# Kernel tuning notes

Hardware: AMD Instinct MI355X
Metric: run time of the kernel (lower is better)

## Reference

```python
import jax, jax.numpy as jnp
import numpy as np

N_LEVELS = 8
BASE_RES = 16
LOG2_T = 14
T = 1 << LOG2_T
WIDTH, HEIGHT = 1024, 768
NUM_GAUSSIAN = 8
PRIME_Y = np.uint32(2654435761)
CORNERS = np.array([[0, 0], [1, 0], [0, 1], [1, 1]], dtype=np.uint32)


def _level_resolutions():
    bx = np.exp((np.log(WIDTH) - np.log(BASE_RES)) / (N_LEVELS - 1))
    by = np.exp((np.log(HEIGHT) - np.log(BASE_RES)) / (N_LEVELS - 1))
    return [(int(np.floor(BASE_RES * bx ** l)), int(np.floor(BASE_RES * by ** l)))
            for l in range(N_LEVELS)]


def hash_encode(x, hashidxs, table):
    # x: [N,2] in [0,1]; hashidxs: [N] int; table: [V, L, T, 2]
    feats = []
    offs = jnp.asarray(CORNERS)  # [4,2] uint32
    hv = hashidxs.astype(jnp.int32)[:, None]  # [N,1]
    for l, (rx, ry) in enumerate(_level_resolutions()):
        res = jnp.array([rx, ry], dtype=x.dtype)
        pos = x * res                      # [N,2]
        p0 = jnp.floor(pos)
        w = pos - p0                       # bilinear weights, [N,2]
        c = p0.astype(jnp.uint32)[:, None, :] + offs[None]  # [N,4,2]
        h = (c[..., 0] * jnp.uint32(1)) ^ (c[..., 1] * PRIME_Y)
        idx = (h & jnp.uint32(T - 1)).astype(jnp.int32)      # [N,4]
        f = table[hv, l, idx]              # [N,4,2] gather per corner
        wx, wy = w[:, 0:1], w[:, 1:2]
        ww = jnp.concatenate([(1 - wx) * (1 - wy), wx * (1 - wy),
                              (1 - wx) * wy, wx * wy], axis=1)  # [N,4]
        feats.append(jnp.sum(f * ww[..., None], axis=1))        # [N,2]
    return jnp.concatenate(feats, axis=-1)  # [N,16]


def gaussian_act(x, sigma=0.1):
    return jnp.exp(x * x * (-1.0 / (2.0 * sigma * sigma)))


def setup_inputs() -> dict:
    key = jax.random.key(0)
    ks = jax.random.split(key, 8)
    N = 2 ** 21
    V = 20
    x = jax.random.uniform(ks[0], (N, 2), dtype=jnp.float32)
    hashidxs = jax.random.randint(ks[1], (N,), 0, V, dtype=jnp.int32)
    color = jax.random.uniform(ks[2], (N, 3), dtype=jnp.float32)
    table = jax.random.normal(ks[3], (V, N_LEVELS, T, 2), dtype=jnp.float32) * 1e-2
    w1 = jax.random.normal(ks[4], (16, 32), dtype=jnp.float32) * (1.0 / np.sqrt(16))
    b1 = jax.random.normal(ks[5], (32,), dtype=jnp.float32) * 0.01
    w2 = jax.random.normal(ks[6], (32, 3 * NUM_GAUSSIAN), dtype=jnp.float32) * (1.0 / np.sqrt(32))
    b2 = jax.random.normal(ks[7], (3 * NUM_GAUSSIAN,), dtype=jnp.float32) * 0.01
    return {"x": x, "hashidxs": hashidxs, "color": color, "table": table,
            "w1": w1, "b1": b1, "w2": w2, "b2": b2}


def reference(x, hashidxs, color, table, w1, b1, w2, b2):
    H = hash_encode(x, hashidxs, table)            # [N,16]
    h1 = gaussian_act(H @ w1 + b1)                 # [N,32]
    raw = h1 @ w2 + b2                             # [N,24]
    G = NUM_GAUSSIAN
    weight = jnp.exp(raw[..., :G])
    mu = jax.nn.sigmoid(raw[..., G:2 * G])
    inv_sigma = jnp.exp(raw[..., 2 * G:3 * G])
    return mu, inv_sigma, weight, H
```

## Files before the change

kernel.cpp:

```cpp
#include <hip/hip_runtime.h>
#include <cmath>

#define NLEV 8
#define TSZ 16384
#define PRIME 2654435761u
#define NBINS 32

typedef float fx2 __attribute__((ext_vector_type(2)));

struct Res { int rx[NLEV]; int ry[NLEV]; };

__device__ __forceinline__ void compute_point(
    fx2 xv, int hv, int p,
    const float* __restrict__ table,
    const float* __restrict__ w1, const float* __restrict__ b1,
    const float* __restrict__ w2, const float* __restrict__ b2,
    float* __restrict__ out, int N, const Res& res)
{
    const float* tb_base = table + (size_t)hv * (NLEV * TSZ * 2);

    float H[16];
    #pragma unroll
    for (int l = 0; l < NLEV; ++l) {
        float fx = (float)res.rx[l], fy = (float)res.ry[l];
        float posx = xv.x * fx, posy = xv.y * fy;
        float p0x = floorf(posx), p0y = floorf(posy);
        float wx = posx - p0x, wy = posy - p0y;
        unsigned cx = (unsigned)p0x, cy = (unsigned)p0y;
        const float* tb = tb_base + (size_t)l * (TSZ * 2);
        unsigned hy0 = cy * PRIME;
        unsigned hy1 = (cy + 1u) * PRIME;
        unsigned i00 = ( cx        ^ hy0) & (TSZ - 1);
        unsigned i10 = ((cx + 1u)  ^ hy0) & (TSZ - 1);
        unsigned i01 = ( cx        ^ hy1) & (TSZ - 1);
        unsigned i11 = ((cx + 1u)  ^ hy1) & (TSZ - 1);
        fx2 f00 = *(const fx2*)(tb + 2u * i00);
        fx2 f10 = *(const fx2*)(tb + 2u * i10);
        fx2 f01 = *(const fx2*)(tb + 2u * i01);
        fx2 f11 = *(const fx2*)(tb + 2u * i11);
        float w00 = (1.f - wx) * (1.f - wy);
        float w10 = wx * (1.f - wy);
        float w01 = (1.f - wx) * wy;
        float w11 = wx * wy;
        H[2*l]   = fmaf(f00.x, w00, fmaf(f10.x, w10, fmaf(f01.x, w01, f11.x * w11)));
        H[2*l+1] = fmaf(f00.y, w00, fmaf(f10.y, w10, fmaf(f01.y, w01, f11.y * w11)));
    }

    float h1[32];
    #pragma unroll
    for (int j = 0; j < 32; ++j) {
        float s = b1[j];
        #pragma unroll
        for (int k = 0; k < 16; ++k) s = fmaf(H[k], w1[k * 32 + j], s);
        h1[j] = __expf(-50.f * s * s);
    }

    float raw[24];
    #pragma unroll
    for (int j = 0; j < 24; ++j) {
        float s = b2[j];
        #pragma unroll
        for (int k = 0; k < 32; ++k) s = fmaf(h1[k], w2[k * 24 + j], s);
        raw[j] = s;
    }

    float wt[8], mu[8], isg[8];
    #pragma unroll
    for (int g = 0; g < 8; ++g) {
        wt[g]  = __expf(raw[g]);
        mu[g]  = 1.f / (1.f + __expf(-raw[8 + g]));
        isg[g] = __expf(raw[16 + g]);
    }

    size_t N8 = (size_t)N * 8;
    float4* o;
    o = (float4*)(out) + (size_t)p * 2;
    o[0] = make_float4(mu[0], mu[1], mu[2], mu[3]);
    o[1] = make_float4(mu[4], mu[5], mu[6], mu[7]);
    o = (float4*)(out + N8) + (size_t)p * 2;
    o[0] = make_float4(isg[0], isg[1], isg[2], isg[3]);
    o[1] = make_float4(isg[4], isg[5], isg[6], isg[7]);
    o = (float4*)(out + 2 * N8) + (size_t)p * 2;
    o[0] = make_float4(wt[0], wt[1], wt[2], wt[3]);
    o[1] = make_float4(wt[4], wt[5], wt[6], wt[7]);
    o = (float4*)(out + 3 * N8) + (size_t)p * 4;
    o[0] = make_float4(H[0],  H[1],  H[2],  H[3]);
    o[1] = make_float4(H[4],  H[5],  H[6],  H[7]);
    o[2] = make_float4(H[8],  H[9],  H[10], H[11]);
    o[3] = make_float4(H[12], H[13], H[14], H[15]);
}

__global__ __launch_bounds__(256) void pg_kernel(
    const float* __restrict__ x, const int* __restrict__ hashidxs,
    const float* __restrict__ table,
    const float* __restrict__ w1, const float* __restrict__ b1,
    const float* __restrict__ w2, const float* __restrict__ b2,
    float* __restrict__ out, int N, Res res)
{
    int i = blockIdx.x * blockDim.x + threadIdx.x;
    if (i >= N) return;
    fx2 xv = ((const fx2*)x)[i];
    int hv = hashidxs[i];
    compute_point(xv, hv, i, table, w1, b1, w2, b2, out, N, res);
}

__global__ void k_zero(int* __restrict__ c) {
    int t = threadIdx.x;
    if (t < 2 * NBINS) c[t] = 0;
}

__global__ __launch_bounds__(256) void k_hist(
    const int* __restrict__ hashidxs, int N, int* __restrict__ hist)
{
    __shared__ int lh[NBINS];
    int t = threadIdx.x;
    if (t < NBINS) lh[t] = 0;
    __syncthreads();
    int i = blockIdx.x * 256 + t;
    if (i < N) atomicAdd(&lh[hashidxs[i]], 1);
    __syncthreads();
    if (t < NBINS && lh[t]) atomicAdd(&hist[t], lh[t]);
}

__global__ void k_scan(const int* __restrict__ hist, int* __restrict__ cursor) {
    if (threadIdx.x == 0 && blockIdx.x == 0) {
        int acc = 0;
        for (int b = 0; b < NBINS; ++b) { cursor[b] = acc; acc += hist[b]; }
    }
}

__global__ __launch_bounds__(256) void k_scatter(
    const float* __restrict__ x, const int* __restrict__ hashidxs, int N,
    int* __restrict__ cursor, int* __restrict__ order, float* __restrict__ sx)
{
    __shared__ int lh[NBINS];
    __shared__ int lbase[NBINS];
    int t = threadIdx.x;
    if (t < NBINS) lh[t] = 0;
    __syncthreads();
    int i = blockIdx.x * 256 + t;
    int hv = -1, r = 0;
    if (i < N) { hv = hashidxs[i]; r = atomicAdd(&lh[hv], 1); }
    __syncthreads();
    if (t < NBINS && lh[t]) lbase[t] = atomicAdd(&cursor[t], lh[t]);
    __syncthreads();
    if (i < N) {
        int pos = lbase[hv] + r;
        order[pos] = i | (hv << 24);
        ((fx2*)sx)[pos] = ((const fx2*)x)[i];
    }
}

__global__ __launch_bounds__(256) void pg_main(
    const int*   __restrict__ order,
    const float* __restrict__ sx,
    const float* __restrict__ table,
    const float* __restrict__ w1, const float* __restrict__ b1,
    const float* __restrict__ w2, const float* __restrict__ b2,
    float* __restrict__ out, int N, Res res)
{
    unsigned nwg  = gridDim.x, orig = blockIdx.x;
    unsigned q = nwg / 8u, rr = nwg % 8u, xcd = orig % 8u;
    unsigned wg = (xcd < rr ? xcd * (q + 1u) : rr * (q + 1u) + (xcd - rr) * q) + orig / 8u;
    int j = (int)(wg * 256u + threadIdx.x);
    if (j >= N) return;

    int packed = order[j];
    int p  = packed & 0xFFFFFF;
    int hv = packed >> 24;
    fx2 xv = ((const fx2*)sx)[j];
    compute_point(xv, hv, p, table, w1, b1, w2, b2, out, N, res);
}

extern "C" void kernel_launch(void* const* d_in, const int* in_sizes, int n_in,
                              void* d_out, int out_size, void* d_ws, size_t ws_size,
                              hipStream_t stream) {
    const float* x        = (const float*)d_in[0];
    const int*   hashidxs = (const int*)  d_in[1];
    const float* table    = (const float*)d_in[3];
    const float* w1       = (const float*)d_in[4];
    const float* b1       = (const float*)d_in[5];
    const float* w2       = (const float*)d_in[6];
    const float* b2       = (const float*)d_in[7];
    float* out = (float*)d_out;
    int N = in_sizes[0] / 2;

    Res res;
    double bx = std::exp((std::log((double)1024) - std::log((double)16)) / 7.0);
    double by = std::exp((std::log((double)768)  - std::log((double)16)) / 7.0);
    for (int l = 0; l < NLEV; ++l) {
        res.rx[l] = (int)std::floor(16.0 * std::pow(bx, (double)l));
        res.ry[l] = (int)std::floor(16.0 * std::pow(by, (double)l));
    }

    dim3 block(256);
    unsigned nwg = (unsigned)((N + 255) / 256);
    dim3 grid(nwg);

    size_t order_off = 1024;
    size_t sx_off    = order_off + (((size_t)N * 4 + 255) & ~(size_t)255);
    size_t ws_need   = sx_off + (size_t)N * 8;

    if (ws_size < ws_need || N >= (1 << 24)) {
        hipLaunchKernelGGL(pg_kernel, grid, block, 0, stream,
                           x, hashidxs, table, w1, b1, w2, b2, out, N, res);
        return;
    }

    int*   hist   = (int*)d_ws;
    int*   cursor = (int*)d_ws + NBINS;
    int*   order  = (int*)((char*)d_ws + order_off);
    float* sx     = (float*)((char*)d_ws + sx_off);

    hipLaunchKernelGGL(k_zero,    dim3(1),   dim3(64),  0, stream, hist);
    hipLaunchKernelGGL(k_hist,    grid,      block,     0, stream, hashidxs, N, hist);
    hipLaunchKernelGGL(k_scan,    dim3(1),   dim3(32),  0, stream, hist, cursor);
    hipLaunchKernelGGL(k_scatter, grid,      block,     0, stream, x, hashidxs, N, cursor, order, sx);
    hipLaunchKernelGGL(pg_main,   grid,      block,     0, stream,
                       order, sx, table, w1, b1, w2, b2, out, N, res);
}
```

Before: 832.3 us.

## Sort points by hash table and spatial cell; pack MLP FMAs

Points were sorted only by hash-table index. They are now binned by table index and a 16x16 spatial cell, so neighbouring threads gather nearby hash-table entries and get better cache reuse. The histogram, scan and scatter kernels are generalised to thousands of bins, using dynamic LDS and a parallel block scan. The two MLP layers now use two-wide vector FMAs so the compiler can emit packed fp32 instructions. The cost is larger LDS use and more global atomics in the sort kernels.

```diff
diff --git a/kernel.cpp b/kernel.cpp
--- a/kernel.cpp
+++ b/kernel.cpp
@@ -4,7 +4,8 @@
 #define NLEV 8
 #define TSZ 16384
 #define PRIME 2654435761u
-#define NBINS 32
+#define CELLS 256
+#define MAXV 32
 
 typedef float fx2 __attribute__((ext_vector_type(2)));
 
@@ -46,23 +47,38 @@
         H[2*l+1] = fmaf(f00.y, w00, fmaf(f10.y, w10, fmaf(f01.y, w01, f11.y * w11)));
     }
 
+    fx2 acc1[16];
+    #pragma unroll
+    for (int j = 0; j < 16; ++j) acc1[j] = ((const fx2*)b1)[j];
+    #pragma unroll
+    for (int k = 0; k < 16; ++k) {
+        fx2 hk = {H[k], H[k]};
+        const fx2* wrow = (const fx2*)(w1 + k * 32);
+        #pragma unroll
+        for (int j = 0; j < 16; ++j)
+            acc1[j] = __builtin_elementwise_fma(hk, wrow[j], acc1[j]);
+    }
     float h1[32];
     #pragma unroll
-    for (int j = 0; j < 32; ++j) {
-        float s = b1[j];
+    for (int j = 0; j < 16; ++j) {
+        h1[2*j]   = __expf(-50.f * acc1[j].x * acc1[j].x);
+        h1[2*j+1] = __expf(-50.f * acc1[j].y * acc1[j].y);
+    }
+
+    fx2 acc2[12];
+    #pragma unroll
+    for (int j = 0; j < 12; ++j) acc2[j] = ((const fx2*)b2)[j];
+    #pragma unroll
+    for (int k = 0; k < 32; ++k) {
+        fx2 hk = {h1[k], h1[k]};
+        const fx2* wrow = (const fx2*)(w2 + k * 24);
         #pragma unroll
-        for (int k = 0; k < 16; ++k) s = fmaf(H[k], w1[k * 32 + j], s);
-        h1[j] = __expf(-50.f * s * s);
-    }
-
+        for (int j = 0; j < 12; ++j)
+            acc2[j] = __builtin_elementwise_fma(hk, wrow[j], acc2[j]);
+    }
     float raw[24];
     #pragma unroll
-    for (int j = 0; j < 24; ++j) {
-        float s = b2[j];
-        #pragma unroll
-        for (int k = 0; k < 32; ++k) s = fmaf(h1[k], w2[k * 24 + j], s);
-        raw[j] = s;
-    }
+    for (int j = 0; j < 12; ++j) { raw[2*j] = acc2[j].x; raw[2*j+1] = acc2[j].y; }
 
     float wt[8], mu[8], isg[8];
     #pragma unroll
@@ -104,50 +120,94 @@
     compute_point(xv, hv, i, table, w1, b1, w2, b2, out, N, res);
 }
 
-__global__ void k_zero(int* __restrict__ c) {
+__device__ __forceinline__ int spatial_bin(fx2 xv, int hv) {
+    int gx = (int)(xv.x * 16.f); gx = gx > 15 ? 15 : gx;
+    int gy = (int)(xv.y * 16.f); gy = gy > 15 ? 15 : gy;
+    return hv * CELLS + gy * 16 + gx;
+}
+
+__global__ __launch_bounds__(256) void k_zero(int* __restrict__ c, int n) {
+    int t = blockIdx.x * 256 + threadIdx.x;
+    if (t < n) c[t] = 0;
+}
+
+__global__ __launch_bounds__(256) void k_hist(
+    const float* __restrict__ x, const int* __restrict__ hashidxs, int N,
+    int* __restrict__ hist, int NB)
+{
+    extern __shared__ int lh[];
+    for (int b = threadIdx.x; b < NB; b += 256) lh[b] = 0;
+    __syncthreads();
+    int i = blockIdx.x * 256 + threadIdx.x;
+    if (i < N) atomicAdd(&lh[spatial_bin(((const fx2*)x)[i], hashidxs[i])], 1);
+    __syncthreads();
+    for (int b = threadIdx.x; b < NB; b += 256) {
+        int c = lh[b];
+        if (c) atomicAdd(&hist[b], c);
+    }
+}
+
+__global__ __launch_bounds__(256) void k_scan(
+    const int* __restrict__ hist, int* __restrict__ cursor, int NB)
+{
+    __shared__ int part[256];
     int t = threadIdx.x;
-    if (t < 2 * NBINS) c[t] = 0;
-}
-
-__global__ __launch_bounds__(256) void k_hist(
-    const int* __restrict__ hashidxs, int N, int* __restrict__ hist)
-{
-    __shared__ int lh[NBINS];
-    int t = threadIdx.x;
-    if (t < NBINS) lh[t] = 0;
-    __syncthreads();
-    int i = blockIdx.x * 256 + t;
-    if (i < N) atomicAdd(&lh[hashidxs[i]], 1);
-    __syncthreads();
-    if (t < NBINS && lh[t]) atomicAdd(&hist[t], lh[t]);
-}
-
-__global__ void k_scan(const int* __restrict__ hist, int* __restrict__ cursor) {
-    if (threadIdx.x == 0 && blockIdx.x == 0) {
-        int acc = 0;
-        for (int b = 0; b < NBINS; ++b) { cursor[b] = acc; acc += hist[b]; }
+    const int BPT = 32;
+    int loc[BPT];
+    int base = t * ((NB + 255) / 256);
+    int cnt  = (NB + 255) / 256;
+    int s = 0;
+    for (int b = 0; b < cnt; ++b) {
+        int bin = base + b;
+        loc[b] = s;
+        if (bin < NB) s += hist[bin];
+    }
+    part[t] = s;
+    __syncthreads();
+    #pragma unroll
+    for (int off = 1; off < 256; off <<= 1) {
+        int v = (t >= off) ? part[t - off] : 0;
+        __syncthreads();
+        part[t] += v;
+        __syncthreads();
+    }
+    int excl = (t == 0) ? 0 : part[t - 1];
+    for (int b = 0; b < cnt; ++b) {
+        int bin = base + b;
+        if (bin < NB) cursor[bin] = excl + loc[b];
     }
 }
 
 __global__ __launch_bounds__(256) void k_scatter(
     const float* __restrict__ x, const int* __restrict__ hashidxs, int N,
-    int* __restrict__ cursor, int* __restrict__ order, float* __restrict__ sx)
-{
-    __shared__ int lh[NBINS];
-    __shared__ int lbase[NBINS];
+    int* __restrict__ cursor, int* __restrict__ order, float* __restrict__ sx,
+    int NB)
+{
+    extern __shared__ int sm[];
+    int* lh    = sm;
+    int* lbase = sm + NB;
     int t = threadIdx.x;
-    if (t < NBINS) lh[t] = 0;
+    for (int b = t; b < NB; b += 256) lh[b] = 0;
     __syncthreads();
     int i = blockIdx.x * 256 + t;
-    int hv = -1, r = 0;
-    if (i < N) { hv = hashidxs[i]; r = atomicAdd(&lh[hv], 1); }
-    __syncthreads();
-    if (t < NBINS && lh[t]) lbase[t] = atomicAdd(&cursor[t], lh[t]);
-    __syncthreads();
+    int bin = -1, r = 0, hv = 0;
+    fx2 xv;
     if (i < N) {
-        int pos = lbase[hv] + r;
+        hv = hashidxs[i];
+        xv = ((const fx2*)x)[i];
+        bin = spatial_bin(xv, hv);
+        r = atomicAdd(&lh[bin], 1);
+    }
+    __syncthreads();
+    for (int b = t; b < NB; b += 256) {
+        int c = lh[b];
+        if (c) lbase[b] = atomicAdd(&cursor[b], c);
+    }
+    __syncthreads();
+    if (i < N) {
+        int pos = lbase[bin] + r;
         order[pos] = i | (hv << 24);
-        ((fx2*)sx)[pos] = ((const fx2*)x)[i];
+        ((fx2*)sx)[pos] = xv;
     }
 }
 
@@ -184,6 +244,7 @@
     const float* b2       = (const float*)d_in[7];
     float* out = (float*)d_out;
     int N = in_sizes[0] / 2;
+    int V = in_sizes[3] / (NLEV * TSZ * 2);
 
     Res res;
     double bx = std::exp((std::log((double)1024) - std::log((double)16)) / 7.0);
@@ -197,25 +258,30 @@
     unsigned nwg = (unsigned)((N + 255) / 256);
     dim3 grid(nwg);
 
-    size_t order_off = 1024;
+    int NB = V * CELLS;
+    size_t order_off = (((size_t)NB * 2 * 4) + 255) & ~(size_t)255;
     size_t sx_off    = order_off + (((size_t)N * 4 + 255) & ~(size_t)255);
     size_t ws_need   = sx_off + (size_t)N * 8;
 
-    if (ws_size < ws_need || N >= (1 << 24)) {
+    if (ws_size < ws_need || N >= (1 << 24) || V <= 0 || V > MAXV) {
         hipLaunchKernelGGL(pg_kernel, grid, block, 0, stream,
                            x, hashidxs, table, w1, b1, w2, b2, out, N, res);
         return;
     }
 
     int*   hist   = (int*)d_ws;
-    int*   cursor = (int*)d_ws + NBINS;
+    int*   cursor = (int*)d_ws + NB;
     int*   order  = (int*)((char*)d_ws + order_off);
     float* sx     = (float*)((char*)d_ws + sx_off);
 
-    hipLaunchKernelGGL(k_zero,    dim3(1),   dim3(64),  0, stream, hist);
-    hipLaunchKernelGGL(k_hist,    grid,      block,     0, stream, hashidxs, N, hist);
-    hipLaunchKernelGGL(k_scan,    dim3(1),   dim3(32),  0, stream, hist, cursor);
-    hipLaunchKernelGGL(k_scatter, grid,      block,     0, stream, x, hashidxs, N, cursor, order, sx);
-    hipLaunchKernelGGL(pg_main,   grid,      block,     0, stream,
+    size_t lds_h = (size_t)NB * 4;
+    size_t lds_s = (size_t)NB * 8;
+
+    hipLaunchKernelGGL(k_zero, dim3((NB + 255) / 256), block, 0, stream, hist, NB);
+    hipLaunchKernelGGL(k_hist, grid, block, lds_h, stream, x, hashidxs, N, hist, NB);
+    hipLaunchKernelGGL(k_scan, dim3(1), block, 0, stream, hist, cursor, NB);
+    hipLaunchKernelGGL(k_scatter, grid, block, lds_s, stream,
+                       x, hashidxs, N, cursor, order, sx, NB);
+    hipLaunchKernelGGL(pg_main, grid, block, 0, stream,
                        order, sx, table, w1, b1, w2, b2, out, N, res);
 }
```

After: 831.5 us. No clear change (-0.1%).
